# Optimization experiments

Measured on AMD Instinct MI355X. Metric: run time of the kernel, lower is better.

Reference implementation:

```python
import jax, jax.numpy as jnp
import numpy as np

B, H, W, C = 4, 128, 128, 256
HEADS, DHEAD = 8, 32


def conv2d(x, w, b=None, groups=1, pad=0):
    # x: [N,C,H,W], w: [O, C//groups, kh, kw]
    out = jax.lax.conv_general_dilated(
        x, w, window_strides=(1, 1), padding=[(pad, pad), (pad, pad)],
        dimension_numbers=("NCHW", "OIHW", "NCHW"), feature_group_count=groups)
    if b is not None:
        out = out + b[None, :, None, None]
    return out


def setup_inputs() -> dict:
    key = jax.random.key(0)
    ks = jax.random.split(key, 16)
    g = lambda i, shape, s=0.02: jax.random.normal(ks[i], shape, jnp.float32) * s
    return {
        "x": jax.random.normal(ks[0], (B, H, W, C), jnp.float32),
        "mask": jax.random.uniform(ks[1], (1, C, H, W), jnp.float32),
        "wq": g(2, (C, C)),
        "wk": g(3, (C, C)),
        "wv": g(4, (C, C)),
        "rescale": jnp.ones((HEADS, 1, 1), jnp.float32),
        "wproj": g(5, (C, C)),
        "bproj": jnp.zeros((C,), jnp.float32),
        "mg_w1": g(6, (C, C, 1, 1)),
        "mg_b1": jnp.zeros((C,), jnp.float32),
        "mg_w2": g(7, (C, C, 1, 1)),
        "mg_b2": jnp.zeros((C,), jnp.float32),
        "mg_dw": g(8, (C, 1, 5, 5)),
        "mg_db": jnp.zeros((C,), jnp.float32),
        "be_w1": g(9, (C, 1, 3, 3)),
        "be_w2": g(10, (C, 1, 3, 3)),
    }


def _l2norm(t, axis):
    n = jnp.sqrt(jnp.sum(t * t, axis=axis, keepdims=True))
    return t / jnp.maximum(n, 1e-12)


def reference(x, mask, wq, wk, wv, rescale, wproj, bproj,
              mg_w1, mg_b1, mg_w2, mg_b2, mg_dw, mg_db, be_w1, be_w2):
    b, h, w, c = x.shape
    heads = rescale.shape[0]
    d = c // heads
    n = h * w

    xf = x.reshape(b, n, c)
    q_inp = xf @ wq   # [b,n,c]
    k_inp = xf @ wk
    v_inp = xf @ wv

    # MaskGuidedMechanism (h==w so shift_back is identity)
    m = conv2d(mask, mg_w1, mg_b1)                                   # [1,c,h,w]
    attn_map = jax.nn.sigmoid(conv2d(conv2d(m, mg_w2, mg_b2), mg_dw, mg_db, groups=c, pad=2))
    m = m * attn_map + m
    mask_emb = jnp.transpose(m, (0, 2, 3, 1))                        # [1,h,w,c]
    ma = jnp.broadcast_to(mask_emb, (b, h, w, c)).reshape(b, n, c)

    split = lambda t: t.reshape(b, n, heads, d).transpose(0, 2, 1, 3)  # [b,heads,n,d]
    q, k, v, ma = map(split, (q_inp, k_inp, v_inp, ma))
    v = v * ma

    # channel attention: normalize over token dim n
    qn = _l2norm(q, axis=2)
    kn = _l2norm(k, axis=2)
    attn = jnp.einsum("bhni,bhnj->bhij", kn, qn)                     # [b,heads,d,d]
    attn = jax.nn.softmax(attn * rescale, axis=-1)
    out = jnp.einsum("bhij,bhnj->bhin", attn, v)                     # [b,heads,d,n]

    out = out.transpose(0, 3, 1, 2).reshape(b, n, heads * d)         # [b,n,c]
    out_c = (out @ wproj + bproj).reshape(b, h, w, c)

    # band_emb: depthwise3x3 -> GELU(exact) -> depthwise3x3 on v_inp image
    v_img = v_inp.reshape(b, h, w, c).transpose(0, 3, 1, 2)          # [b,c,h,w]
    y = conv2d(v_img, be_w1, groups=c, pad=1)
    y = jax.nn.gelu(y, approximate=False)
    y = conv2d(y, be_w2, groups=c, pad=1)
    out_p = y.transpose(0, 2, 3, 1)

    return out_c + out_p
```

## Files before the change

kernel.cpp:

```cpp
#include <hip/hip_runtime.h>
#include <stdint.h>

#define B 4
#define HW 128
#define C 256
#define NTOK 16384
#define MALL 65536
#define HEADS 8
#define DH 32

typedef float f32x4 __attribute__((ext_vector_type(4)));
typedef short s16x8 __attribute__((ext_vector_type(8)));
typedef short s16x4 __attribute__((ext_vector_type(4)));
typedef __bf16 bf16x8 __attribute__((ext_vector_type(8)));

__device__ __forceinline__ float bf2f(unsigned short u) {
  union { unsigned int i; float f; } x;
  x.i = ((unsigned int)u) << 16;
  return x.f;
}
__device__ __forceinline__ unsigned short f2bf(float f) {
  union { float f; unsigned int i; } x;
  x.f = f;
  unsigned int lsb = (x.i >> 16) & 1u;
  unsigned int r = x.i + 0x7fffu + lsb;
  return (unsigned short)(r >> 16);
}

__device__ __forceinline__ void gload_lds16(const void* g, void* l) {
  auto gp = reinterpret_cast<const __attribute__((address_space(1))) unsigned int*>(
      reinterpret_cast<uintptr_t>(g));
  auto lp = reinterpret_cast<__attribute__((address_space(3))) unsigned int*>(
      reinterpret_cast<uintptr_t>(l));
  __builtin_amdgcn_global_load_lds(gp, lp, 16, 0, 0);
}

#define CFENCE asm volatile("" ::: "memory")
#define LDSBAR()                                        \
  do {                                                  \
    asm volatile("s_waitcnt lgkmcnt(0)" ::: "memory");  \
    __builtin_amdgcn_s_barrier();                       \
    CFENCE;                                             \
  } while (0)

__global__ __launch_bounds__(256) void prep_w_kernel(
    const float* __restrict__ wq, const float* __restrict__ wk, const float* __restrict__ wv,
    const float* __restrict__ wproj, const float* __restrict__ w1, const float* __restrict__ w2,
    unsigned short* __restrict__ wqkvT, unsigned short* __restrict__ wprojT,
    unsigned short* __restrict__ w1b, unsigned short* __restrict__ w2b) {
  const int idx = blockIdx.x * 256 + threadIdx.x;
  const int mat = blockIdx.y;
  const int n = idx >> 8, k = idx & 255;
  switch (mat) {
    case 0: wqkvT[idx] = f2bf(wq[k * 256 + n]); break;
    case 1: wqkvT[65536 + idx] = f2bf(wk[k * 256 + n]); break;
    case 2: wqkvT[131072 + idx] = f2bf(wv[k * 256 + n]); break;
    case 3: wprojT[idx] = f2bf(wproj[k * 256 + n]); break;
    case 4: w1b[idx] = f2bf(w1[idx]); break;
    case 5: w2b[idx] = f2bf(w2[idx]); break;
  }
}

__global__ __launch_bounds__(1024) void tmask_kernel(const float* __restrict__ mask,
                                                     unsigned short* __restrict__ mT) {
  __shared__ float tile[32][33];
  const int p0 = blockIdx.x * 32, c0 = blockIdx.y * 32;
  const int tx = threadIdx.x & 31, ty = threadIdx.x >> 5;
  tile[ty][tx] = mask[(size_t)(c0 + ty) * NTOK + p0 + tx];
  __syncthreads();
  mT[(size_t)(p0 + ty) * C + c0 + tx] = f2bf(tile[tx][ty]);
}

__global__ __launch_bounds__(256) void gemm128_qkv_kernel(
    const float* __restrict__ X, const unsigned short* __restrict__ Bt,
    unsigned short* __restrict__ q, unsigned short* __restrict__ k,
    unsigned short* __restrict__ v) {
  __shared__ alignas(16) unsigned short smem[16384];
  const int nwg = gridDim.x;
  const int bid = blockIdx.x;
  const int qd = nwg >> 3, rr = nwg & 7;
  const int xcd = bid & 7, sidx = bid >> 3;
  const int swz = (xcd < rr ? xcd * (qd + 1) : rr * (qd + 1) + (xcd - rr) * qd) + sidx;
  const int m0 = (swz / 6) * 128;
  const int n0 = (swz % 6) * 128;
  const int t = threadIdx.x;
  const int w = t >> 6, l = t & 63;
  const int wr = w >> 1, wc = w & 1;
  const int lr = l & 15, lg = l >> 4;

  const int r = t >> 1;
  const int rm3 = r & 3;
  const int p0s = (((t & 1) * 2 + 0) ^ rm3);
  const int p1s = (((t & 1) * 2 + 1) ^ rm3);
  const int br = t >> 2;
  const int bsl = (t & 3) ^ (br & 3);

  f32x4 va0, va1, va2, va3;
  auto ALOAD = [&](int kt) {
    const float* src = X + (size_t)(m0 + r) * 256 + kt * 32;
    va0 = *(const f32x4*)(src + p0s * 8);
    va1 = *(const f32x4*)(src + p0s * 8 + 4);
    va2 = *(const f32x4*)(src + p1s * 8);
    va3 = *(const f32x4*)(src + p1s * 8 + 4);
  };
  auto AWRITE = [&](int buf) {
    s16x8 o0, o1;
#pragma unroll
    for (int e = 0; e < 4; ++e) {
      o0[e] = (short)f2bf(va0[e]);
      o0[e + 4] = (short)f2bf(va1[e]);
      o1[e] = (short)f2bf(va2[e]);
      o1[e + 4] = (short)f2bf(va3[e]);
    }
    unsigned short* d = smem + buf * 4096 + t * 16;
    *(s16x8*)d = o0;
    *(s16x8*)(d + 8) = o1;
  };
  auto STAGEB = [&](int kt, int buf) {
    char* dbase = (char*)(smem + 8192 + buf * 4096);
    gload_lds16(Bt + (size_t)(n0 + br) * 256 + kt * 32 + bsl * 8, dbase + t * 16);
    gload_lds16(Bt + (size_t)(n0 + 64 + br) * 256 + kt * 32 + bsl * 8,
                dbase + 4096 + t * 16);
  };

  f32x4 acc[4][4];
#pragma unroll
  for (int i = 0; i < 4; ++i)
#pragma unroll
    for (int j = 0; j < 4; ++j) acc[i][j] = f32x4{0.f, 0.f, 0.f, 0.f};

  const int fsl = (lg ^ (lr & 3)) * 8;

  ALOAD(0);
  STAGEB(0, 0);
  asm volatile("s_waitcnt vmcnt(0)" ::: "memory");
  AWRITE(0);
  LDSBAR();

#pragma unroll
  for (int kt = 0; kt < 8; ++kt) {
    const int cur = kt & 1;
    if (kt < 7) {
      ALOAD(kt + 1);
      STAGEB(kt + 1, cur ^ 1);
    }
    bf16x8 af[4], bfv[4];
#pragma unroll
    for (int j = 0; j < 4; ++j)
      bfv[j] = *(const bf16x8*)&smem[8192 + cur * 4096 + (wc * 64 + j * 16 + lr) * 32 + fsl];
#pragma unroll
    for (int i = 0; i < 4; ++i)
      af[i] = *(const bf16x8*)&smem[cur * 4096 + (wr * 64 + i * 16 + lr) * 32 + fsl];
    __builtin_amdgcn_s_setprio(1);
#pragma unroll
    for (int i = 0; i < 4; ++i)
#pragma unroll
      for (int j = 0; j < 4; ++j)
        acc[i][j] = __builtin_amdgcn_mfma_f32_16x16x32_bf16(af[i], bfv[j], acc[i][j], 0, 0, 0);
    __builtin_amdgcn_s_setprio(0);
    if (kt < 7) {
      asm volatile("s_waitcnt vmcnt(0)" ::: "memory");
      AWRITE(cur ^ 1);
    }
    LDSBAR();
  }

  unsigned short* dstp = (n0 < 256) ? q : (n0 < 512 ? k : v);
  const int cbase = n0 & 255;
  unsigned short* eph = smem;
#pragma unroll
  for (int c = 0; c < 2; ++c) {
    if (c) LDSBAR();
    if (wr == c) {
#pragma unroll
      for (int i = 0; i < 4; ++i) {
        const int lbase = i * 16 + lg * 4;
#pragma unroll
        for (int j = 0; j < 4; ++j) {
          const int col = wc * 64 + j * 16 + lr;
#pragma unroll
          for (int r2 = 0; r2 < 4; ++r2) eph[(lbase + r2) * 136 + col] = f2bf(acc[i][j][r2]);
        }
      }
    }
    LDSBAR();
#pragma unroll
    for (int c2 = 0; c2 < 4; ++c2) {
      const int lrow = c2 * 16 + (t >> 4);
      const s16x8 vv = *(const s16x8*)&eph[lrow * 136 + (t & 15) * 8];
      *(s16x8*)&dstp[(size_t)(m0 + c * 64 + lrow) * C + cbase + (t & 15) * 8] = vv;
    }
  }
}

__global__ __launch_bounds__(256) void gemm128_proj_kernel(
    const unsigned short* __restrict__ V, const unsigned short* __restrict__ memb,
    const unsigned short* __restrict__ weff, const float* __restrict__ bias,
    const unsigned short* __restrict__ y2, float* __restrict__ out) {
  __shared__ alignas(16) unsigned short smem[16384];
  const int nwg = gridDim.x;
  const int bid = blockIdx.x;
  const int qd = nwg >> 3, rr = nwg & 7;
  const int xcd = bid & 7, sidx = bid >> 3;
  const int swz = (xcd < rr ? xcd * (qd + 1) : rr * (qd + 1) + (xcd - rr) * qd) + sidx;
  const int m0 = (swz >> 1) * 128;
  const int n0 = (swz & 1) * 128;
  const unsigned short* Bt = weff + (size_t)(m0 >> 14) * 65536;
  const int t = threadIdx.x;
  const int w = t >> 6, l = t & 63;
  const int wr = w >> 1, wc = w & 1;
  const int lr = l & 15, lg = l >> 4;

  const int r = t >> 1;
  const int rm3 = r & 3;
  const int p0s = (((t & 1) * 2 + 0) ^ rm3);
  const int p1s = (((t & 1) * 2 + 1) ^ rm3);
  const size_t mrow = (size_t)((m0 & 16383) + r);
  const int br = t >> 2;
  const int bsl = (t & 3) ^ (br & 3);

  s16x8 va0, va1, ma0, ma1;
  auto ALOAD = [&](int kt) {
    const unsigned short* vsrc = V + (size_t)(m0 + r) * 256 + kt * 32;
    const unsigned short* msrc = memb + mrow * 256 + kt * 32;
    va0 = *(const s16x8*)(vsrc + p0s * 8);
    ma0 = *(const s16x8*)(msrc + p0s * 8);
    va1 = *(const s16x8*)(vsrc + p1s * 8);
    ma1 = *(const s16x8*)(msrc + p1s * 8);
  };
  auto AWRITE = [&](int buf) {
    s16x8 o0, o1;
#pragma unroll
    for (int e = 0; e < 8; ++e) {
      o0[e] = (short)f2bf(bf2f((unsigned short)va0[e]) * bf2f((unsigned short)ma0[e]));
      o1[e] = (short)f2bf(bf2f((unsigned short)va1[e]) * bf2f((unsigned short)ma1[e]));
    }
    unsigned short* d = smem + buf * 4096 + t * 16;
    *(s16x8*)d = o0;
    *(s16x8*)(d + 8) = o1;
  };
  auto STAGEB = [&](int kt, int buf) {
    char* dbase = (char*)(smem + 8192 + buf * 4096);
    gload_lds16(Bt + (size_t)(n0 + br) * 256 + kt * 32 + bsl * 8, dbase + t * 16);
    gload_lds16(Bt + (size_t)(n0 + 64 + br) * 256 + kt * 32 + bsl * 8,
                dbase + 4096 + t * 16);
  };

  f32x4 acc[4][4];
#pragma unroll
  for (int i = 0; i < 4; ++i)
#pragma unroll
    for (int j = 0; j < 4; ++j) acc[i][j] = f32x4{0.f, 0.f, 0.f, 0.f};

  const int fsl = (lg ^ (lr & 3)) * 8;

  ALOAD(0);
  STAGEB(0, 0);
  asm volatile("s_waitcnt vmcnt(0)" ::: "memory");
  AWRITE(0);
  LDSBAR();

#pragma unroll
  for (int kt = 0; kt < 8; ++kt) {
    const int cur = kt & 1;
    if (kt < 7) {
      ALOAD(kt + 1);
      STAGEB(kt + 1, cur ^ 1);
    }
    bf16x8 af[4], bfv[4];
#pragma unroll
    for (int j = 0; j < 4; ++j)
      bfv[j] = *(const bf16x8*)&smem[8192 + cur * 4096 + (wc * 64 + j * 16 + lr) * 32 + fsl];
#pragma unroll
    for (int i = 0; i < 4; ++i)
      af[i] = *(const bf16x8*)&smem[cur * 4096 + (wr * 64 + i * 16 + lr) * 32 + fsl];
    __builtin_amdgcn_s_setprio(1);
#pragma unroll
    for (int i = 0; i < 4; ++i)
#pragma unroll
      for (int j = 0; j < 4; ++j)
        acc[i][j] = __builtin_amdgcn_mfma_f32_16x16x32_bf16(af[i], bfv[j], acc[i][j], 0, 0, 0);
    __builtin_amdgcn_s_setprio(0);
    if (kt < 7) {
      asm volatile("s_waitcnt vmcnt(0)" ::: "memory");
      AWRITE(cur ^ 1);
    }
    LDSBAR();
  }

  float* ephf = (float*)smem;
  const int colc = t & 31;
  const int trow = t >> 5;
  const int gc4 = n0 + colc * 4;
  const f32x4 bv = *(const f32x4*)&bias[gc4];
#pragma unroll
  for (int c = 0; c < 4; ++c) {
    if (c) LDSBAR();
    if (wr == (c >> 1)) {
#pragma unroll
      for (int b2 = 0; b2 < 2; ++b2) {
        const int ii = (c & 1) * 2 + b2;
        const int lbase = b2 * 16 + lg * 4;
#pragma unroll
        for (int j = 0; j < 4; ++j) {
          const int col = wc * 64 + j * 16 + lr;
#pragma unroll
          for (int r2 = 0; r2 < 4; ++r2) ephf[(lbase + r2) * 132 + col] = acc[ii][j][r2];
        }
      }
    }
    LDSBAR();
#pragma unroll
    for (int c2 = 0; c2 < 4; ++c2) {
      const int lrow = c2 * 8 + trow;
      const int grow = m0 + c * 32 + lrow;
      const f32x4 vv = *(const f32x4*)&ephf[lrow * 132 + colc * 4];
      const s16x4 yv = *(const s16x4*)&y2[(size_t)grow * C + gc4];
      f32x4 o;
#pragma unroll
      for (int e = 0; e < 4; ++e) o[e] = vv[e] + bv[e] + bf2f((unsigned short)yv[e]);
      *(f32x4*)&out[(size_t)grow * C + gc4] = o;
    }
  }
}

__global__ __launch_bounds__(256) void gemm_bt_kernel(
    const unsigned short* __restrict__ A, const unsigned short* __restrict__ Bt, const int K,
    const int nbn, const int mode, unsigned short* __restrict__ ob0,
    unsigned short* __restrict__ ob1, unsigned short* __restrict__ ob2,
    const float* __restrict__ bias, float* __restrict__ of32) {
  __shared__ unsigned short lA[2][128 * 64];
  __shared__ unsigned short lB[2][128 * 64];
  const int nwg = gridDim.x;
  const int bid = blockIdx.x;
  const int qd = nwg >> 3, rr = nwg & 7;
  const int xcd = bid & 7, sidx = bid >> 3;
  const int swz = (xcd < rr ? xcd * (qd + 1) : rr * (qd + 1) + (xcd - rr) * qd) + sidx;
  const int m0 = (swz / nbn) * 128;
  const int n0 = (swz % nbn) * 128;
  const int t = threadIdx.x;
  const int w = t >> 6, l = t & 63;
  const int wr = w >> 1, wc = w & 1;
  const int lr = l & 15, lg = l >> 4;

  const int strow = (l >> 3);
  const int scolb = (((l & 7) ^ strow) << 4);

  f32x4 acc[4][4];
#pragma unroll
  for (int i = 0; i < 4; ++i)
#pragma unroll
    for (int j = 0; j < 4; ++j) acc[i][j] = f32x4{0.f, 0.f, 0.f, 0.f};

  auto stage = [&](int buf, int k0) {
#pragma unroll
    for (int s = 0; s < 4; ++s) {
      const int seg = w * 4 + s;
      const int row = seg * 8 + strow;
      gload_lds16((const char*)A + ((size_t)(m0 + row) * K + k0) * 2 + scolb,
                  (char*)&lA[buf][0] + seg * 1024 + (l & 7) * 16);
      gload_lds16((const char*)Bt + ((size_t)(n0 + row) * K + k0) * 2 + scolb,
                  (char*)&lB[buf][0] + seg * 1024 + (l & 7) * 16);
    }
  };
  auto compute = [&](int buf) {
#pragma unroll
    for (int kk = 0; kk < 64; kk += 32) {
      bf16x8 af[4], bfr[4];
      const int sbase = (kk >> 3) + lg;
      const int p = (sbase ^ (lr & 7)) << 3;
#pragma unroll
      for (int i = 0; i < 4; ++i)
        af[i] = *(const bf16x8*)&lA[buf][(wr * 64 + i * 16 + lr) * 64 + p];
#pragma unroll
      for (int j = 0; j < 4; ++j)
        bfr[j] = *(const bf16x8*)&lB[buf][(wc * 64 + j * 16 + lr) * 64 + p];
#pragma unroll
      for (int i = 0; i < 4; ++i)
#pragma unroll
        for (int j = 0; j < 4; ++j)
          acc[i][j] = __builtin_amdgcn_mfma_f32_16x16x32_bf16(af[i], bfr[j], acc[i][j], 0, 0, 0);
    }
  };

  stage(0, 0);
  __syncthreads();
  int cur = 0;
  for (int k0 = 64; k0 < K; k0 += 64) {
    stage(cur ^ 1, k0);
    compute(cur);
    __syncthreads();
    cur ^= 1;
  }
  compute(cur);

#pragma unroll
  for (int i = 0; i < 4; ++i) {
    const int grow = m0 + wr * 64 + i * 16 + lg * 4;
#pragma unroll
    for (int j = 0; j < 4; ++j) {
      const int gcol = n0 + wc * 64 + j * 16 + lr;
#pragma unroll
      for (int r = 0; r < 4; ++r) {
        const float v = acc[i][j][r];
        const size_t row = (size_t)(grow + r);
        if (mode == 0) {
          unsigned short* dst = (gcol < 256) ? ob0 : (gcol < 512 ? ob1 : ob2);
          dst[row * C + (gcol & 255)] = f2bf(v);
        } else if (mode == 1) {
          ob0[row * C + gcol] = f2bf(v + bias[gcol]);
        } else {
          const size_t idx = row * C + gcol;
          of32[idx] += v + bias[gcol];
        }
      }
    }
  }
}

__global__ __launch_bounds__(256) void mask_dw5_kernel(
    const unsigned short* __restrict__ m2, const unsigned short* __restrict__ m1,
    const float* __restrict__ dw, const float* __restrict__ db,
    unsigned short* __restrict__ memb) {
  __shared__ float wlds[25 * 256];
  __shared__ float blds[256];
  const int t = threadIdx.x;
  const int y = blockIdx.y;
  const int x0 = blockIdx.x * 16 + (t >> 6) * 4;
  const int cg = (t & 63) * 4;
#pragma unroll
  for (int e = 0; e < 25; ++e) wlds[e * 256 + t] = dw[t * 25 + e];
  blds[t] = db[t];
  __syncthreads();

  const f32x4 bias = *(const f32x4*)&blds[cg];
  f32x4 acc[4];
#pragma unroll
  for (int xi = 0; xi < 4; ++xi) acc[xi] = bias;

#pragma unroll
  for (int dy = 0; dy < 5; ++dy) {
    const int yy = y + dy - 2;
    if (yy < 0 || yy >= HW) continue;
    f32x4 col[8];
#pragma unroll
    for (int j = 0; j < 8; ++j) {
      const int xx = x0 - 2 + j;
      if (xx >= 0 && xx < HW) {
        const s16x4 v = *(const s16x4*)&m2[((size_t)yy * HW + xx) * C + cg];
        col[j][0] = bf2f((unsigned short)v[0]);
        col[j][1] = bf2f((unsigned short)v[1]);
        col[j][2] = bf2f((unsigned short)v[2]);
        col[j][3] = bf2f((unsigned short)v[3]);
      } else {
        col[j] = f32x4{0.f, 0.f, 0.f, 0.f};
      }
    }
#pragma unroll
    for (int dx = 0; dx < 5; ++dx) {
      const f32x4 wv = *(const f32x4*)&wlds[(dy * 5 + dx) * 256 + cg];
#pragma unroll
      for (int xi = 0; xi < 4; ++xi) acc[xi] += wv * col[dx + xi];
    }
  }

#pragma unroll
  for (int xi = 0; xi < 4; ++xi) {
    const size_t oi = ((size_t)y * HW + x0 + xi) * C + cg;
    const s16x4 mv = *(const s16x4*)&m1[oi];
    s16x4 o;
#pragma unroll
    for (int ch = 0; ch < 4; ++ch) {
      const float a = 1.f / (1.f + __expf(-acc[xi][ch]));
      o[ch] = (short)f2bf(bf2f((unsigned short)mv[ch]) * (1.f + a));
    }
    *(s16x4*)&memb[oi] = o;
  }
}

__global__ __launch_bounds__(256) void gram_kernel(const unsigned short* __restrict__ qb,
                                                   const unsigned short* __restrict__ kb,
                                                   float* __restrict__ Gpart,
                                                   float* __restrict__ ssq,
                                                   float* __restrict__ ssk) {
  const int chunk = blockIdx.x;
  const int h = blockIdx.y;
  const int b = blockIdx.z;
  __shared__ float flk[128 * 32], flq[128 * 32];
  const int t = threadIdx.x;
  const int wv = t >> 6;
  const int i0 = (t & 7) * 4, j0 = ((t >> 3) & 7) * 4;
  const int lrow = t >> 2, lcb = (t & 3) * 8;
  float acc[4][4] = {};
  float sq[8] = {}, sk[8] = {};
  for (int sub = 0; sub < 8; ++sub) {
    const size_t nbase = (size_t)b * NTOK + chunk * 1024 + sub * 128;
    __syncthreads();
#pragma unroll
    for (int it = 0; it < 2; ++it) {
      const int row = it * 64 + lrow;
      const s16x8 kv8 = *(const s16x8*)&kb[(nbase + row) * C + h * 32 + lcb];
      const s16x8 qv8 = *(const s16x8*)&qb[(nbase + row) * C + h * 32 + lcb];
      f32x4 ka, kbb, qa, qbb;
#pragma unroll
      for (int e = 0; e < 4; ++e) {
        ka[e] = bf2f((unsigned short)kv8[e]);
        kbb[e] = bf2f((unsigned short)kv8[e + 4]);
        qa[e] = bf2f((unsigned short)qv8[e]);
        qbb[e] = bf2f((unsigned short)qv8[e + 4]);
      }
#pragma unroll
      for (int e = 0; e < 4; ++e) {
        sk[e] += ka[e] * ka[e];
        sk[e + 4] += kbb[e] * kbb[e];
        sq[e] += qa[e] * qa[e];
        sq[e + 4] += qbb[e] * qbb[e];
      }
      *(f32x4*)&flk[row * 32 + lcb] = ka;
      *(f32x4*)&flk[row * 32 + lcb + 4] = kbb;
      *(f32x4*)&flq[row * 32 + lcb] = qa;
      *(f32x4*)&flq[row * 32 + lcb + 4] = qbb;
    }
    __syncthreads();
    for (int n = wv; n < 128; n += 4) {
      const f32x4 kv = *(const f32x4*)&flk[n * 32 + i0];
      const f32x4 qv = *(const f32x4*)&flq[n * 32 + j0];
#pragma unroll
      for (int a = 0; a < 4; ++a)
#pragma unroll
        for (int bb = 0; bb < 4; ++bb) acc[a][bb] += kv[a] * qv[bb];
    }
  }
  const int pc = chunk * 4 + wv;
  float* dst = Gpart + (((size_t)pc * B + b) * HEADS + h) * 1024;
#pragma unroll
  for (int a = 0; a < 4; ++a)
#pragma unroll
    for (int bb = 0; bb < 4; ++bb) dst[(i0 + a) * 32 + (j0 + bb)] = acc[a][bb];
  __syncthreads();
#pragma unroll
  for (int e = 0; e < 8; ++e) {
    flq[t * 8 + e] = sq[e];
    flk[t * 8 + e] = sk[e];
  }
  __syncthreads();
  if (t < 32) {
    const int tm = t >> 3, e = t & 7;
    float s1 = 0.f, s2 = 0.f;
    for (int k2 = 0; k2 < 64; ++k2) {
      const int tt = tm + k2 * 4;
      s1 += flq[tt * 8 + e];
      s2 += flk[tt * 8 + e];
    }
    ssq[((size_t)b * 16 + chunk) * C + h * 32 + t] = s1;
    ssk[((size_t)b * 16 + chunk) * C + h * 32 + t] = s2;
  }
}

__global__ __launch_bounds__(256) void softmax_kernel(
    const float* __restrict__ Gpart, const float* __restrict__ ssq,
    const float* __restrict__ ssk, const float* __restrict__ rescale,
    unsigned short* __restrict__ attnb) {
  const int h = blockIdx.x, b = blockIdx.y;
  const int t = threadIdx.x;
  __shared__ float G[1024];
  __shared__ float nq[32], nk[32];
#pragma unroll
  for (int e = 0; e < 4; ++e) {
    const int cell = e * 256 + t;
    float s = 0.f;
    for (int pc = 0; pc < 64; ++pc)
      s += Gpart[(((size_t)pc * B + b) * HEADS + h) * 1024 + cell];
    G[cell] = s;
  }
  if (t < 64) {
    const int d = t & 31;
    const float* ss = (t < 32) ? ssq : ssk;
    float s = 0.f;
    for (int ch = 0; ch < 16; ++ch) s += ss[((size_t)b * 16 + ch) * C + h * 32 + d];
    const float nn = fmaxf(sqrtf(s), 1e-12f);
    if (t < 32) nq[d] = nn;
    else nk[d] = nn;
  }
  __syncthreads();
  if (t < 32) {
    const int i = t;
    const float rs = rescale[h];
    float row[32];
    float mx = -1e30f;
#pragma unroll
    for (int j = 0; j < 32; ++j) {
      const float v = G[i * 32 + j] / (nk[i] * nq[j]) * rs;
      row[j] = v;
      mx = fmaxf(mx, v);
    }
    float sum = 0.f;
#pragma unroll
    for (int j = 0; j < 32; ++j) {
      const float e = expf(row[j] - mx);
      row[j] = e;
      sum += e;
    }
    const float inv = 1.f / sum;
#pragma unroll
    for (int j = 0; j < 32; ++j)
      attnb[(((size_t)b * HEADS + h) * 32 + i) * 32 + j] = f2bf(row[j] * inv);
  }
}

__global__ __launch_bounds__(256) void weff_kernel(const unsigned short* __restrict__ attnb,
                                                   const unsigned short* __restrict__ wprojT,
                                                   unsigned short* __restrict__ weff) {
  const int b = blockIdx.y;
  const int co0 = blockIdx.x * 64;
  const int t = threadIdx.x;
  __shared__ float att[8192];
  for (int e = t; e < 8192; e += 256) att[e] = bf2f(attnb[(size_t)b * 8192 + e]);
  __syncthreads();
  const int o = co0 + (t & 63);
  const int hq = t >> 6;
#pragma unroll
  for (int hh = 0; hh < 2; ++hh) {
    const int h = hq * 2 + hh;
    float wp[32];
#pragma unroll
    for (int i = 0; i < 32; ++i) wp[i] = bf2f(wprojT[(size_t)o * 256 + h * 32 + i]);
    for (int j4 = 0; j4 < 8; ++j4) {
      f32x4 s = {0.f, 0.f, 0.f, 0.f};
#pragma unroll
      for (int i = 0; i < 32; ++i) {
        const f32x4 a4 = *(const f32x4*)&att[(h * 32 + i) * 32 + j4 * 4];
        s += wp[i] * a4;
      }
      s16x4 oo;
#pragma unroll
      for (int e = 0; e < 4; ++e) oo[e] = (short)f2bf(s[e]);
      *(s16x4*)&weff[((size_t)b * 256 + o) * 256 + h * 32 + j4 * 4] = oo;
    }
  }
}

__global__ __launch_bounds__(512) void dw3_kernel(const unsigned short* __restrict__ in,
                                                  const float* __restrict__ wgt,
                                                  unsigned short* __restrict__ out_bf,
                                                  const int do_gelu) {
  const int y = blockIdx.x;
  const int b = blockIdx.y;
  const int t = threadIdx.x;
  const int cg = (t & 63) * 4;
  const int x0 = (t >> 6) * 16;
  float w[9][4];
#pragma unroll
  for (int e = 0; e < 9; ++e)
#pragma unroll
    for (int ch = 0; ch < 4; ++ch) w[e][ch] = wgt[(cg + ch) * 9 + e];
  const int ym = y - 1, yp = y + 1;
  const bool hm = (ym >= 0), hp = (yp < HW);
  const size_t base = (size_t)b * NTOK * C + cg;
  auto ld4 = [&](int yy, int xx) -> f32x4 {
    const s16x4 v = *(const s16x4*)&in[base + ((size_t)yy * HW + xx) * C];
    f32x4 f;
    f[0] = bf2f((unsigned short)v[0]);
    f[1] = bf2f((unsigned short)v[1]);
    f[2] = bf2f((unsigned short)v[2]);
    f[3] = bf2f((unsigned short)v[3]);
    return f;
  };
  const f32x4 zero = {0.f, 0.f, 0.f, 0.f};
  f32x4 a0, a1, a2, b0, b1, b2;
  if (x0 > 0) {
    a0 = hm ? ld4(ym, x0 - 1) : zero;
    a1 = ld4(y, x0 - 1);
    a2 = hp ? ld4(yp, x0 - 1) : zero;
  } else {
    a0 = a1 = a2 = zero;
  }
  b0 = hm ? ld4(ym, x0) : zero;
  b1 = ld4(y, x0);
  b2 = hp ? ld4(yp, x0) : zero;
  for (int xi = 0; xi < 16; ++xi) {
    const int x = x0 + xi;
    f32x4 c0, c1, c2;
    if (x + 1 < HW) {
      c0 = hm ? ld4(ym, x + 1) : zero;
      c1 = ld4(y, x + 1);
      c2 = hp ? ld4(yp, x + 1) : zero;
    } else {
      c0 = c1 = c2 = zero;
    }
    float res[4];
#pragma unroll
    for (int ch = 0; ch < 4; ++ch) {
      float r = w[0][ch] * a0[ch] + w[1][ch] * b0[ch] + w[2][ch] * c0[ch] +
                w[3][ch] * a1[ch] + w[4][ch] * b1[ch] + w[5][ch] * c1[ch] +
                w[6][ch] * a2[ch] + w[7][ch] * b2[ch] + w[8][ch] * c2[ch];
      if (do_gelu) r = 0.5f * r * (1.f + erff(r * 0.70710678118654752f));
      res[ch] = r;
    }
    const size_t oi = base + ((size_t)y * HW + x) * C;
    s16x4 o;
    o[0] = (short)f2bf(res[0]);
    o[1] = (short)f2bf(res[1]);
    o[2] = (short)f2bf(res[2]);
    o[3] = (short)f2bf(res[3]);
    *(s16x4*)&out_bf[oi] = o;
    a0 = b0; a1 = b1; a2 = b2;
    b0 = c0; b1 = c1; b2 = c2;
  }
}

extern "C" void kernel_launch(void* const* d_in, const int* in_sizes, int n_in, void* d_out,
                              int out_size, void* d_ws, size_t ws_size, hipStream_t stream) {
  (void)in_sizes; (void)n_in; (void)out_size; (void)ws_size;
  const float* x = (const float*)d_in[0];
  const float* maskp = (const float*)d_in[1];
  const float* wq = (const float*)d_in[2];
  const float* wk = (const float*)d_in[3];
  const float* wv = (const float*)d_in[4];
  const float* rescale = (const float*)d_in[5];
  const float* wproj = (const float*)d_in[6];
  const float* bproj = (const float*)d_in[7];
  const float* mg_w1 = (const float*)d_in[8];
  const float* mg_b1 = (const float*)d_in[9];
  const float* mg_w2 = (const float*)d_in[10];
  const float* mg_b2 = (const float*)d_in[11];
  const float* mg_dw = (const float*)d_in[12];
  const float* mg_db = (const float*)d_in[13];
  const float* be_w1 = (const float*)d_in[14];
  const float* be_w2 = (const float*)d_in[15];
  float* out = (float*)d_out;
  char* ws = (char*)d_ws;

  unsigned short* qb = (unsigned short*)(ws + 33554432ull);
  unsigned short* kb = (unsigned short*)(ws + 67108864ull);
  unsigned short* vb = (unsigned short*)(ws + 100663296ull);
  unsigned short* mT = (unsigned short*)(ws + 134217728ull);
  unsigned short* m1b = (unsigned short*)(ws + 142606336ull);
  unsigned short* m2b = (unsigned short*)(ws + 150994944ull);
  unsigned short* wqkvT = (unsigned short*)(ws + 159383552ull);
  unsigned short* wprojT = (unsigned short*)(ws + 159776768ull);
  unsigned short* w1b = (unsigned short*)(ws + 159907840ull);
  unsigned short* w2b = (unsigned short*)(ws + 160038912ull);
  float* ssq = (float*)(ws + 160169984ull);
  float* ssk = (float*)(ws + 160432128ull);
  unsigned short* attnb = (unsigned short*)(ws + 160694272ull);
  float* Gpart = (float*)m2b;
  unsigned short* memb = mT;
  unsigned short* y1 = qb;
  unsigned short* y2 = kb;
  unsigned short* weff = m1b;

  prep_w_kernel<<<dim3(256, 6), 256, 0, stream>>>(wq, wk, wv, wproj, mg_w1, mg_w2, wqkvT,
                                                  wprojT, w1b, w2b);
  tmask_kernel<<<dim3(512, 8), 1024, 0, stream>>>(maskp, mT);
  gemm_bt_kernel<<<256, 256, 0, stream>>>(mT, w1b, 256, 2, 1, m1b, nullptr, nullptr, mg_b1,
                                          nullptr);
  gemm_bt_kernel<<<256, 256, 0, stream>>>(m1b, w2b, 256, 2, 1, m2b, nullptr, nullptr, mg_b2,
                                          nullptr);
  mask_dw5_kernel<<<dim3(8, 128), 256, 0, stream>>>(m2b, m1b, mg_dw, mg_db, memb);
  gemm128_qkv_kernel<<<3072, 256, 0, stream>>>(x, wqkvT, qb, kb, vb);
  gram_kernel<<<dim3(16, 8, 4), 256, 0, stream>>>(qb, kb, Gpart, ssq, ssk);
  softmax_kernel<<<dim3(8, 4), 256, 0, stream>>>(Gpart, ssq, ssk, rescale, attnb);
  weff_kernel<<<dim3(4, 4), 256, 0, stream>>>(attnb, wprojT, weff);
  dw3_kernel<<<dim3(128, 4), 512, 0, stream>>>(vb, be_w1, y1, 1);
  dw3_kernel<<<dim3(128, 4), 512, 0, stream>>>(y1, be_w2, y2, 0);
  gemm128_proj_kernel<<<1024, 256, 0, stream>>>(vb, memb, weff, bproj, y2, out);
}
```

Before: 315.8 us.

## Enlarge QKV and projection GEMM tiles to 256x256 with 512-thread workgroups

```diff
diff --git a/kernel.cpp b/kernel.cpp
--- a/kernel.cpp
+++ b/kernel.cpp
@@ -71,37 +71,36 @@
   mT[(size_t)(p0 + ty) * C + c0 + tx] = f2bf(tile[tx][ty]);
 }
 
-__global__ __launch_bounds__(256) void gemm128_qkv_kernel(
+__global__ __launch_bounds__(512) void gemm256_qkv_kernel(
     const float* __restrict__ X, const unsigned short* __restrict__ Bt,
     unsigned short* __restrict__ q, unsigned short* __restrict__ k,
     unsigned short* __restrict__ v) {
-  __shared__ alignas(16) unsigned short smem[16384];
+  __shared__ alignas(16) unsigned short smem[32768];
+  unsigned short* lAb = smem;
+  unsigned short* lBb = smem + 16384;
   const int nwg = gridDim.x;
   const int bid = blockIdx.x;
   const int qd = nwg >> 3, rr = nwg & 7;
   const int xcd = bid & 7, sidx = bid >> 3;
   const int swz = (xcd < rr ? xcd * (qd + 1) : rr * (qd + 1) + (xcd - rr) * qd) + sidx;
-  const int m0 = (swz / 6) * 128;
-  const int n0 = (swz % 6) * 128;
+  const int m0 = (swz / 3) * 256;
+  const int n0 = (swz % 3) * 256;
   const int t = threadIdx.x;
   const int w = t >> 6, l = t & 63;
-  const int wr = w >> 1, wc = w & 1;
+  const int wr = w >> 2, wc = w & 3;
   const int lr = l & 15, lg = l >> 4;
 
-  const int r = t >> 1;
-  const int rm3 = r & 3;
-  const int p0s = (((t & 1) * 2 + 0) ^ rm3);
-  const int p1s = (((t & 1) * 2 + 1) ^ rm3);
-  const int br = t >> 2;
-  const int bsl = (t & 3) ^ (br & 3);
+  const int srow = t >> 2;
+  const int ssl = (t & 3) ^ ((t >> 3) & 3);
 
   f32x4 va0, va1, va2, va3;
   auto ALOAD = [&](int kt) {
-    const float* src = X + (size_t)(m0 + r) * 256 + kt * 32;
-    va0 = *(const f32x4*)(src + p0s * 8);
-    va1 = *(const f32x4*)(src + p0s * 8 + 4);
-    va2 = *(const f32x4*)(src + p1s * 8);
-    va3 = *(const f32x4*)(src + p1s * 8 + 4);
+    const float* s0 = X + (size_t)(m0 + srow) * 256 + kt * 32 + ssl * 8;
+    const float* s1 = X + (size_t)(m0 + 128 + srow) * 256 + kt * 32 + ssl * 8;
+    va0 = *(const f32x4*)s0;
+    va1 = *(const f32x4*)(s0 + 4);
+    va2 = *(const f32x4*)s1;
+    va3 = *(const f32x4*)(s1 + 4);
   };
   auto AWRITE = [&](int buf) {
     s16x8 o0, o1;
@@ -112,24 +111,28 @@
       o1[e] = (short)f2bf(va2[e]);
       o1[e + 4] = (short)f2bf(va3[e]);
     }
-    unsigned short* d = smem + buf * 4096 + t * 16;
-    *(s16x8*)d = o0;
-    *(s16x8*)(d + 8) = o1;
+    char* d = (char*)(lAb + buf * 8192);
+    *(s16x8*)(d + t * 16) = o0;
+    *(s16x8*)(d + 8192 + t * 16) = o1;
   };
   auto STAGEB = [&](int kt, int buf) {
-    char* dbase = (char*)(smem + 8192 + buf * 4096);
-    gload_lds16(Bt + (size_t)(n0 + br) * 256 + kt * 32 + bsl * 8, dbase + t * 16);
-    gload_lds16(Bt + (size_t)(n0 + 64 + br) * 256 + kt * 32 + bsl * 8,
-                dbase + 4096 + t * 16);
-  };
-
-  f32x4 acc[4][4];
-#pragma unroll
-  for (int i = 0; i < 4; ++i)
-#pragma unroll
-    for (int j = 0; j < 4; ++j) acc[i][j] = f32x4{0.f, 0.f, 0.f, 0.f};
-
-  const int fsl = (lg ^ (lr & 3)) * 8;
+    unsigned short* d = lBb + buf * 8192;
+    const size_t kb = ((size_t)kt * 32 + ssl * 8) * 2;
+    gload_lds16((const char*)Bt + ((size_t)(n0 + srow) * 256) * 2 + kb, (char*)d + t * 16);
+    gload_lds16((const char*)Bt + ((size_t)(n0 + 128 + srow) * 256) * 2 + kb,
+                (char*)d + 8192 + t * 16);
+  };
+
+  f32x4 acc[8][4];
+#pragma unroll
+  for (int m = 0; m < 8; ++m)
+#pragma unroll
+    for (int j = 0; j < 4; ++j) acc[m][j] = f32x4{0.f, 0.f, 0.f, 0.f};
+
+  const int asl = (lg ^ ((lr >> 1) & 3)) * 8;
+  const int aoff = lr * 32 + asl;
+  const int awb = wr * 4096;
+  const int boff = (wc >> 1) * 4096 + ((wc & 1) * 64 + lr) * 32 + asl;
 
   ALOAD(0);
   STAGEB(0, 0);
@@ -140,23 +143,31 @@
 #pragma unroll
   for (int kt = 0; kt < 8; ++kt) {
     const int cur = kt & 1;
+    const unsigned short* bufA = lAb + cur * 8192;
+    const unsigned short* bufB = lBb + cur * 8192;
+    bf16x8 bfr[4], af[4], af2[4];
+#pragma unroll
+    for (int j = 0; j < 4; ++j) bfr[j] = *(const bf16x8*)&bufB[boff + j * 512];
+#pragma unroll
+    for (int m = 0; m < 4; ++m) af[m] = *(const bf16x8*)&bufA[awb + aoff + m * 512];
+#pragma unroll
+    for (int m = 0; m < 4; ++m) af2[m] = *(const bf16x8*)&bufA[awb + aoff + (m + 4) * 512];
     if (kt < 7) {
       ALOAD(kt + 1);
       STAGEB(kt + 1, cur ^ 1);
     }
-    bf16x8 af[4], bfv[4];
-#pragma unroll
-    for (int j = 0; j < 4; ++j)
-      bfv[j] = *(const bf16x8*)&smem[8192 + cur * 4096 + (wc * 64 + j * 16 + lr) * 32 + fsl];
-#pragma unroll
-    for (int i = 0; i < 4; ++i)
-      af[i] = *(const bf16x8*)&smem[cur * 4096 + (wr * 64 + i * 16 + lr) * 32 + fsl];
     __builtin_amdgcn_s_setprio(1);
 #pragma unroll
-    for (int i = 0; i < 4; ++i)
+    for (int m = 0; m < 4; ++m)
 #pragma unroll
       for (int j = 0; j < 4; ++j)
-        acc[i][j] = __builtin_amdgcn_mfma_f32_16x16x32_bf16(af[i], bfv[j], acc[i][j], 0, 0, 0);
+        acc[m][j] = __builtin_amdgcn_mfma_f32_16x16x32_bf16(af[m], bfr[j], acc[m][j], 0, 0, 0);
+#pragma unroll
+    for (int m = 0; m < 4; ++m)
+#pragma unroll
+      for (int j = 0; j < 4; ++j)
+        acc[m + 4][j] =
+            __builtin_amdgcn_mfma_f32_16x16x32_bf16(af2[m], bfr[j], acc[m + 4][j], 0, 0, 0);
     __builtin_amdgcn_s_setprio(0);
     if (kt < 7) {
       asm volatile("s_waitcnt vmcnt(0)" ::: "memory");
@@ -165,68 +176,66 @@
     LDSBAR();
   }
 
-  unsigned short* dstp = (n0 < 256) ? q : (n0 < 512 ? k : v);
-  const int cbase = n0 & 255;
+  unsigned short* dst = (n0 < 256) ? q : (n0 < 512 ? k : v);
   unsigned short* eph = smem;
 #pragma unroll
-  for (int c = 0; c < 2; ++c) {
-    if (c) LDSBAR();
-    if (wr == c) {
-#pragma unroll
-      for (int i = 0; i < 4; ++i) {
-        const int lbase = i * 16 + lg * 4;
+  for (int c = 0; c < 4; ++c) {
+    LDSBAR();
+    if (wr == (c >> 1)) {
+#pragma unroll
+      for (int mm = 0; mm < 4; ++mm) {
+        const int m = (c & 1) * 4 + mm;
+        const int lrow = mm * 16 + lg * 4;
 #pragma unroll
         for (int j = 0; j < 4; ++j) {
           const int col = wc * 64 + j * 16 + lr;
 #pragma unroll
-          for (int r2 = 0; r2 < 4; ++r2) eph[(lbase + r2) * 136 + col] = f2bf(acc[i][j][r2]);
+          for (int r = 0; r < 4; ++r) eph[(lrow + r) * 264 + col] = f2bf(acc[m][j][r]);
         }
       }
     }
     LDSBAR();
+    const int col16 = t & 31;
 #pragma unroll
     for (int c2 = 0; c2 < 4; ++c2) {
-      const int lrow = c2 * 16 + (t >> 4);
-      const s16x8 vv = *(const s16x8*)&eph[lrow * 136 + (t & 15) * 8];
-      *(s16x8*)&dstp[(size_t)(m0 + c * 64 + lrow) * C + cbase + (t & 15) * 8] = vv;
-    }
-  }
-}
-
-__global__ __launch_bounds__(256) void gemm128_proj_kernel(
+      const int lrow = c2 * 16 + (t >> 5);
+      const int grow = m0 + c * 64 + lrow;
+      const s16x8 vv = *(const s16x8*)&eph[lrow * 264 + col16 * 8];
+      *(s16x8*)&dst[(size_t)grow * C + col16 * 8] = vv;
+    }
+  }
+}
+
+__global__ __launch_bounds__(512) void gemm256_proj_kernel(
     const unsigned short* __restrict__ V, const unsigned short* __restrict__ memb,
     const unsigned short* __restrict__ weff, const float* __restrict__ bias,
     const unsigned short* __restrict__ y2, float* __restrict__ out) {
-  __shared__ alignas(16) unsigned short smem[16384];
+  __shared__ alignas(16) unsigned short smem[32768];
+  unsigned short* lAb = smem;
+  unsigned short* lBb = smem + 16384;
   const int nwg = gridDim.x;
   const int bid = blockIdx.x;
   const int qd = nwg >> 3, rr = nwg & 7;
   const int xcd = bid & 7, sidx = bid >> 3;
   const int swz = (xcd < rr ? xcd * (qd + 1) : rr * (qd + 1) + (xcd - rr) * qd) + sidx;
-  const int m0 = (swz >> 1) * 128;
-  const int n0 = (swz & 1) * 128;
+  const int m0 = swz * 256;
   const unsigned short* Bt = weff + (size_t)(m0 >> 14) * 65536;
   const int t = threadIdx.x;
   const int w = t >> 6, l = t & 63;
-  const int wr = w >> 1, wc = w & 1;
+  const int wr = w >> 2, wc = w & 3;
   const int lr = l & 15, lg = l >> 4;
 
-  const int r = t >> 1;
-  const int rm3 = r & 3;
-  const int p0s = (((t & 1) * 2 + 0) ^ rm3);
-  const int p1s = (((t & 1) * 2 + 1) ^ rm3);
-  const size_t mrow = (size_t)((m0 & 16383) + r);
-  const int br = t >> 2;
-  const int bsl = (t & 3) ^ (br & 3);
+  const int srow = t >> 2;
+  const int ssl = (t & 3) ^ ((t >> 3) & 3);
+  const size_t mrow = (size_t)((m0 & 16383) + srow);
 
   s16x8 va0, va1, ma0, ma1;
   auto ALOAD = [&](int kt) {
-    const unsigned short* vsrc = V + (size_t)(m0 + r) * 256 + kt * 32;
-    const unsigned short* msrc = memb + mrow * 256 + kt * 32;
-    va0 = *(const s16x8*)(vsrc + p0s * 8);
-    ma0 = *(const s16x8*)(msrc + p0s * 8);
-    va1 = *(const s16x8*)(vsrc + p1s * 8);
-    ma1 = *(const s16x8*)(msrc + p1s * 8);
+    const int ko = kt * 32 + ssl * 8;
+    va0 = *(const s16x8*)&V[(size_t)(m0 + srow) * 256 + ko];
+    ma0 = *(const s16x8*)&memb[mrow * 256 + ko];
+    va1 = *(const s16x8*)&V[(size_t)(m0 + 128 + srow) * 256 + ko];
+    ma1 = *(const s16x8*)&memb[(mrow + 128) * 256 + ko];
   };
   auto AWRITE = [&](int buf) {
     s16x8 o0, o1;
@@ -235,24 +244,28 @@
       o0[e] = (short)f2bf(bf2f((unsigned short)va0[e]) * bf2f((unsigned short)ma0[e]));
       o1[e] = (short)f2bf(bf2f((unsigned short)va1[e]) * bf2f((unsigned short)ma1[e]));
     }
-    unsigned short* d = smem + buf * 4096 + t * 16;
-    *(s16x8*)d = o0;
-    *(s16x8*)(d + 8) = o1;
+    char* d = (char*)(lAb + buf * 8192);
+    *(s16x8*)(d + t * 16) = o0;
+    *(s16x8*)(d + 8192 + t * 16) = o1;
   };
   auto STAGEB = [&](int kt, int buf) {
-    char* dbase = (char*)(smem + 8192 + buf * 4096);
-    gload_lds16(Bt + (size_t)(n0 + br) * 256 + kt * 32 + bsl * 8, dbase + t * 16);
-    gload_lds16(Bt + (size_t)(n0 + 64 + br) * 256 + kt * 32 + bsl * 8,
-                dbase + 4096 + t * 16);
-  };
-
-  f32x4 acc[4][4];
-#pragma unroll
-  for (int i = 0; i < 4; ++i)
-#pragma unroll
-    for (int j = 0; j < 4; ++j) acc[i][j] = f32x4{0.f, 0.f, 0.f, 0.f};
-
-  const int fsl = (lg ^ (lr & 3)) * 8;
+    unsigned short* d = lBb + buf * 8192;
+    const size_t kb = ((size_t)kt * 32 + ssl * 8) * 2;
+    gload_lds16((const char*)Bt + ((size_t)srow * 256) * 2 + kb, (char*)d + t * 16);
+    gload_lds16((const char*)Bt + ((size_t)(128 + srow) * 256) * 2 + kb,
+                (char*)d + 8192 + t * 16);
+  };
+
+  f32x4 acc[8][4];
+#pragma unroll
+  for (int m = 0; m < 8; ++m)
+#pragma unroll
+    for (int j = 0; j < 4; ++j) acc[m][j] = f32x4{0.f, 0.f, 0.f, 0.f};
+
+  const int asl = (lg ^ ((lr >> 1) & 3)) * 8;
+  const int aoff = lr * 32 + asl;
+  const int awb = wr * 4096;
+  const int boff = (wc >> 1) * 4096 + ((wc & 1) * 64 + lr) * 32 + asl;
 
   ALOAD(0);
   STAGEB(0, 0);
@@ -263,23 +276,31 @@
 #pragma unroll
   for (int kt = 0; kt < 8; ++kt) {
     const int cur = kt & 1;
+    const unsigned short* bufA = lAb + cur * 8192;
+    const unsigned short* bufB = lBb + cur * 8192;
+    bf16x8 bfr[4], af[4], af2[4];
+#pragma unroll
+    for (int j = 0; j < 4; ++j) bfr[j] = *(const bf16x8*)&bufB[boff + j * 512];
+#pragma unroll
+    for (int m = 0; m < 4; ++m) af[m] = *(const bf16x8*)&bufA[awb + aoff + m * 512];
+#pragma unroll
+    for (int m = 0; m < 4; ++m) af2[m] = *(const bf16x8*)&bufA[awb + aoff + (m + 4) * 512];
     if (kt < 7) {
       ALOAD(kt + 1);
       STAGEB(kt + 1, cur ^ 1);
     }
-    bf16x8 af[4], bfv[4];
-#pragma unroll
-    for (int j = 0; j < 4; ++j)
-      bfv[j] = *(const bf16x8*)&smem[8192 + cur * 4096 + (wc * 64 + j * 16 + lr) * 32 + fsl];
-#pragma unroll
-    for (int i = 0; i < 4; ++i)
-      af[i] = *(const bf16x8*)&smem[cur * 4096 + (wr * 64 + i * 16 + lr) * 32 + fsl];
     __builtin_amdgcn_s_setprio(1);
 #pragma unroll
-    for (int i = 0; i < 4; ++i)
+    for (int m = 0; m < 4; ++m)
 #pragma unroll
       for (int j = 0; j < 4; ++j)
-        acc[i][j] = __builtin_amdgcn_mfma_f32_16x16x32_bf16(af[i], bfv[j], acc[i][j], 0, 0, 0);
+        acc[m][j] = __builtin_amdgcn_mfma_f32_16x16x32_bf16(af[m], bfr[j], acc[m][j], 0, 0, 0);
+#pragma unroll
+    for (int m = 0; m < 4; ++m)
+#pragma unroll
+      for (int j = 0; j < 4; ++j)
+        acc[m + 4][j] =
+            __builtin_amdgcn_mfma_f32_16x16x32_bf16(af2[m], bfr[j], acc[m + 4][j], 0, 0, 0);
     __builtin_amdgcn_s_setprio(0);
     if (kt < 7) {
       asm volatile("s_waitcnt vmcnt(0)" ::: "memory");
@@ -289,37 +310,35 @@
   }
 
   float* ephf = (float*)smem;
-  const int colc = t & 31;
-  const int trow = t >> 5;
-  const int gc4 = n0 + colc * 4;
-  const f32x4 bv = *(const f32x4*)&bias[gc4];
-#pragma unroll
-  for (int c = 0; c < 4; ++c) {
-    if (c) LDSBAR();
-    if (wr == (c >> 1)) {
-#pragma unroll
-      for (int b2 = 0; b2 < 2; ++b2) {
-        const int ii = (c & 1) * 2 + b2;
-        const int lbase = b2 * 16 + lg * 4;
+  const int colc = t & 63;
+  const f32x4 bv = *(const f32x4*)&bias[colc * 4];
+#pragma unroll
+  for (int c = 0; c < 8; ++c) {
+    LDSBAR();
+    if (wr == (c >> 2)) {
+#pragma unroll
+      for (int mm = 0; mm < 2; ++mm) {
+        const int m = (c & 3) * 2 + mm;
+        const int lrow = mm * 16 + lg * 4;
 #pragma unroll
         for (int j = 0; j < 4; ++j) {
           const int col = wc * 64 + j * 16 + lr;
 #pragma unroll
-          for (int r2 = 0; r2 < 4; ++r2) ephf[(lbase + r2) * 132 + col] = acc[ii][j][r2];
+          for (int r = 0; r < 4; ++r) ephf[(lrow + r) * 260 + col] = acc[m][j][r];
         }
       }
     }
     LDSBAR();
 #pragma unroll
     for (int c2 = 0; c2 < 4; ++c2) {
-      const int lrow = c2 * 8 + trow;
+      const int lrow = c2 * 8 + (t >> 6);
       const int grow = m0 + c * 32 + lrow;
-      const f32x4 vv = *(const f32x4*)&ephf[lrow * 132 + colc * 4];
-      const s16x4 yv = *(const s16x4*)&y2[(size_t)grow * C + gc4];
+      const f32x4 vv = *(const f32x4*)&ephf[lrow * 260 + colc * 4];
+      const s16x4 yv = *(const s16x4*)&y2[(size_t)grow * C + colc * 4];
       f32x4 o;
 #pragma unroll
       for (int e = 0; e < 4; ++e) o[e] = vv[e] + bv[e] + bf2f((unsigned short)yv[e]);
-      *(f32x4*)&out[(size_t)grow * C + gc4] = o;
+      *(f32x4*)&out[(size_t)grow * C + colc * 4] = o;
     }
   }
 }
@@ -327,8 +346,7 @@
 __global__ __launch_bounds__(256) void gemm_bt_kernel(
     const unsigned short* __restrict__ A, const unsigned short* __restrict__ Bt, const int K,
     const int nbn, const int mode, unsigned short* __restrict__ ob0,
-    unsigned short* __restrict__ ob1, unsigned short* __restrict__ ob2,
-    const float* __restrict__ bias, float* __restrict__ of32) {
+    const float* __restrict__ bias) {
   __shared__ unsigned short lA[2][128 * 64];
   __shared__ unsigned short lB[2][128 * 64];
   const int nwg = gridDim.x;
@@ -404,15 +422,7 @@
       for (int r = 0; r < 4; ++r) {
         const float v = acc[i][j][r];
         const size_t row = (size_t)(grow + r);
-        if (mode == 0) {
-          unsigned short* dst = (gcol < 256) ? ob0 : (gcol < 512 ? ob1 : ob2);
-          dst[row * C + (gcol & 255)] = f2bf(v);
-        } else if (mode == 1) {
-          ob0[row * C + gcol] = f2bf(v + bias[gcol]);
-        } else {
-          const size_t idx = row * C + gcol;
-          of32[idx] += v + bias[gcol];
-        }
+        ob0[row * C + gcol] = f2bf(v + bias[gcol]);
       }
     }
   }
@@ -753,16 +763,14 @@
   prep_w_kernel<<<dim3(256, 6), 256, 0, stream>>>(wq, wk, wv, wproj, mg_w1, mg_w2, wqkvT,
                                                   wprojT, w1b, w2b);
   tmask_kernel<<<dim3(512, 8), 1024, 0, stream>>>(maskp, mT);
-  gemm_bt_kernel<<<256, 256, 0, stream>>>(mT, w1b, 256, 2, 1, m1b, nullptr, nullptr, mg_b1,
-                                          nullptr);
-  gemm_bt_kernel<<<256, 256, 0, stream>>>(m1b, w2b, 256, 2, 1, m2b, nullptr, nullptr, mg_b2,
-                                          nullptr);
+  gemm_bt_kernel<<<256, 256, 0, stream>>>(mT, w1b, 256, 2, 1, m1b, mg_b1);
+  gemm_bt_kernel<<<256, 256, 0, stream>>>(m1b, w2b, 256, 2, 1, m2b, mg_b2);
   mask_dw5_kernel<<<dim3(8, 128), 256, 0, stream>>>(m2b, m1b, mg_dw, mg_db, memb);
-  gemm128_qkv_kernel<<<3072, 256, 0, stream>>>(x, wqkvT, qb, kb, vb);
+  gemm256_qkv_kernel<<<768, 512, 0, stream>>>(x, wqkvT, qb, kb, vb);
   gram_kernel<<<dim3(16, 8, 4), 256, 0, stream>>>(qb, kb, Gpart, ssq, ssk);
   softmax_kernel<<<dim3(8, 4), 256, 0, stream>>>(Gpart, ssq, ssk, rescale, attnb);
   weff_kernel<<<dim3(4, 4), 256, 0, stream>>>(attnb, wprojT, weff);
   dw3_kernel<<<dim3(128, 4), 512, 0, stream>>>(vb, be_w1, y1, 1);
   dw3_kernel<<<dim3(128, 4), 512, 0, stream>>>(y1, be_w2, y2, 0);
-  gemm128_proj_kernel<<<1024, 256, 0, stream>>>(vb, memb, weff, bproj, y2, out);
-}
+  gemm256_proj_kernel<<<256, 512, 0, stream>>>(vb, memb, weff, bproj, y2, out);
+}
```

After: 278.1 us. 11.9% less time.
